# Performance work log

Hardware: AMD Instinct MI355X
Metric: run time of the kernel (lower is better)

The kernel has to match this reference:

```python
import jax, jax.numpy as jnp
import numpy as np

B, T, I, H = 64, 512, 512, 1024


def setup_inputs() -> dict:
    key = jax.random.key(0)
    ks = jax.random.split(key, 14)
    s = 0.05
    d = {"x": jax.random.normal(ks[0], (B, T, I), dtype=jnp.float32)}
    names = ["W_i", "W_f", "W_c", "W_o"]
    for n, k in zip(names, ks[1:5]):
        d[n] = jax.random.normal(k, (H, I), dtype=jnp.float32) * s
    for n, k in zip(["U_i", "U_f", "U_c", "U_o"], ks[5:9]):
        d[n] = jax.random.normal(k, (H, H), dtype=jnp.float32) * s
    for n, k in zip(["b_i", "b_f", "b_c", "b_o"], ks[9:13]):
        d[n] = jax.random.normal(k, (H,), dtype=jnp.float32) * s
    return d


def _lstm(x, W_i, W_f, W_c, W_o, b_i, b_f, b_c, b_o, U_i, U_f, U_c, U_o):
    # Precompute all input-gate preactivations in big GEMMs: (B,T,H)
    xi = jnp.einsum("bti,hi->bth", x, W_i) + b_i
    xf = jnp.einsum("bti,hi->bth", x, W_f) + b_f
    xg = jnp.einsum("bti,hi->bth", x, W_c) + b_c
    xo = jnp.einsum("bti,hi->bth", x, W_o) + b_o
    # time-major for scan: (T,B,H)
    xs = (xi.transpose(1, 0, 2), xf.transpose(1, 0, 2),
          xg.transpose(1, 0, 2), xo.transpose(1, 0, 2))
    h0 = jnp.zeros((x.shape[0], U_i.shape[0]), dtype=x.dtype)
    c0 = jnp.zeros_like(h0)

    def step(carry, xt):
        h, c = carry
        xi_t, xf_t, xg_t, xo_t = xt
        i = jax.nn.sigmoid(xi_t + h @ U_i.T)
        f = jax.nn.sigmoid(xf_t + h @ U_f.T)
        g = jnp.tanh(xg_t + h @ U_c.T)
        o = jax.nn.sigmoid(xo_t + h @ U_o.T)
        c_n = f * c + i * g
        h_n = o * jnp.tanh(c_n)
        return (h_n, c_n), h_n

    (h_n, c_n), ys = jax.lax.scan(step, (h0, c0), xs)
    out = ys.transpose(1, 0, 2)  # (B,T,H), batch_first
    return out, h_n, c_n


def reference(x, W_i, W_f, W_c, W_o, U_i, U_f, U_c, U_o, b_i, b_f, b_c, b_o):
    return _lstm(x, W_i, W_f, W_c, W_o, b_i, b_f, b_c, b_o, U_i, U_f, U_c, U_o)
```

## Files before the change

kernel.cpp:

```cpp
#include <hip/hip_runtime.h>
#include <hip/hip_bf16.h>


typedef __attribute__((ext_vector_type(8))) short bf16x8;
typedef __attribute__((ext_vector_type(4))) float f32x4;
typedef unsigned int uint32;

static __device__ __forceinline__ unsigned short f2bf(float f) {
    union { float f; unsigned int u; } v; v.f = f;
    unsigned int r = v.u + 0x7fffu + ((v.u >> 16) & 1u);
    return (unsigned short)(r >> 16);
}

#define NB   64
#define NT   512
#define NI   512
#define NH   1024
#define NWG  64


__global__ void prep_fast(const float* __restrict__ x,
                          const float* __restrict__ Wi, const float* __restrict__ Wf,
                          const float* __restrict__ Wc, const float* __restrict__ Wo,
                          unsigned short* __restrict__ Wb, unsigned short* __restrict__ xTb,
                          uint32* __restrict__ hb, int* __restrict__ arr)
{
    const int NW  = 4 * NH * NI;
    const int NX  = NB * NT * NI;
    const int NHB = 2 * NB * (NH / 2);
    const int total = NW + NX + NHB + NT;
    for (int idx = blockIdx.x * blockDim.x + threadIdx.x; idx < total;
         idx += gridDim.x * blockDim.x) {
        if (idx < NW) {
            int g = idx >> 19;
            int off = idx & 524287;
            const float* W = (g == 0) ? Wi : (g == 1) ? Wf : (g == 2) ? Wc : Wo;
            Wb[idx] = f2bf(W[off]);
        } else if (idx < NW + NX) {
            int e = idx - NW;
            int b = e >> 18;
            int r = e & 262143;
            int t = r >> 9;
            int i = r & 511;
            xTb[((size_t)t * NB + b) * NI + i] = f2bf(x[e]);
        } else if (idx < NW + NX + NHB) {
            hb[idx - NW - NX] = 0;
        } else {
            arr[idx - NW - NX - NHB] = 0;
        }
    }
}

__global__ __launch_bounds__(1024) void lstm_persist(
    const float* __restrict__ Ui, const float* __restrict__ Uf,
    const float* __restrict__ Uc, const float* __restrict__ Uo,
    const float* __restrict__ b_i, const float* __restrict__ b_f,
    const float* __restrict__ b_c, const float* __restrict__ b_o,
    const unsigned short* __restrict__ Wb, const unsigned short* __restrict__ xT,
    uint32* __restrict__ hb0, uint32* __restrict__ hb1,
    int* __restrict__ arr,
    float* __restrict__ out, float* __restrict__ hn_arr, float* __restrict__ cn_arr)
{
    __shared__ __align__(16) unsigned char smem[163840];
    unsigned char* Us   = smem;
    unsigned char* stg0 = smem + 131072;
    unsigned char* stg1 = smem + 147456;
    float* gacc = (float*)(smem + 131072);

    const int tid  = threadIdx.x;
    const int lane = tid & 63;
    const int wv   = tid >> 6;
    const int g    = wv & 3;
    const int mt   = wv >> 2;
    const int rm   = lane & 15;
    const int kg   = (lane >> 4) * 8;
    const int u0   = blockIdx.x * 16;

    for (int i = 0; i < 8; ++i) {
        int unit = i * 1024 + tid;
        int row  = unit >> 7;
        int k0   = (unit & 127) * 8;
        int gg   = row >> 4;
        const float* src = (gg == 0 ? Ui : gg == 1 ? Uf : gg == 2 ? Uc : Uo)
                           + (size_t)(u0 + (row & 15)) * NH + k0;
        bf16x8 v;
        #pragma unroll
        for (int j = 0; j < 8; ++j) v[j] = (short)f2bf(src[j]);
        *(bf16x8*)(Us + row * 2048 + ((k0 * 2) ^ ((row & 15) << 4))) = v;
    }

    const int bl = tid >> 4, ul = tid & 15;
    const float rbi = b_i[u0 + ul], rbf = b_f[u0 + ul];
    const float rbc = b_c[u0 + ul], rbo = b_o[u0 + ul];
    float creg = 0.f;

    const int sb   = bl;
    const int k8   = ul * 8;
    const int soff = sb * 256 + ((k8 * 2) ^ ((sb & 15) << 4));
    const size_t hrow = (size_t)sb * (NH / 2);

    const int abase = (mt * 16 + rm) * 256;
    const int ubase = (g * 16 + rm) * 2048;
    const size_t wrow = ((size_t)(g * NH + u0 + rm)) * NI;

    __syncthreads();

    for (int t = 0; t < NT; ++t) {
        const uint32* hin = (t & 1) ? hb1 : hb0;
        uint32* hout      = (t & 1) ? hb0 : hb1;
        const unsigned short* xrow = xT + ((size_t)t * NB + sb) * NI;

        f32x4 acc = {0.f, 0.f, 0.f, 0.f};
        uint32 rr[4][4];

        #pragma unroll
        for (int c = 0; c < 4; ++c) {
            uint32* hp = (uint32*)(hin + hrow + (c * 128 + k8) / 2);
            #pragma unroll
            for (int j = 0; j < 4; ++j)
                rr[c][j] = __hip_atomic_load(hp + j, __ATOMIC_RELAXED,
                                             __HIP_MEMORY_SCOPE_AGENT);
        }
        {
            uint4 v; v.x = rr[0][0]; v.y = rr[0][1]; v.z = rr[0][2]; v.w = rr[0][3];
            *(uint4*)(stg0 + soff) = v;
        }
        __syncthreads();

        #pragma unroll
        for (int c = 0; c < 12; ++c) {
            if (c + 4 < 12) {
                const int cc = c + 4;
                if (cc < 8) {
                    uint32* hp = (uint32*)(hin + hrow + (cc * 128 + k8) / 2);
                    #pragma unroll
                    for (int j = 0; j < 4; ++j)
                        rr[cc & 3][j] = __hip_atomic_load(hp + j, __ATOMIC_RELAXED,
                                                          __HIP_MEMORY_SCOPE_AGENT);
                } else {
                    const uint4 v = *(const uint4*)(xrow + (cc - 8) * 128 + k8);
                    rr[cc & 3][0] = v.x; rr[cc & 3][1] = v.y;
                    rr[cc & 3][2] = v.z; rr[cc & 3][3] = v.w;
                }
            }
            const unsigned char* sbuf = (c & 1) ? stg1 : stg0;
            #pragma unroll
            for (int kk = 0; kk < 4; ++kk) {
                const int kloc = kk * 32 + kg;
                bf16x8 af = *(const bf16x8*)(sbuf + abase + ((kloc * 2) ^ (rm << 4)));
                bf16x8 bfg;
                if (c < 8) {
                    const int kglob = c * 128 + kloc;
                    bfg = *(const bf16x8*)(Us + ubase + ((kglob * 2) ^ (rm << 4)));
                } else {
                    bfg = *(const bf16x8*)(Wb + wrow + (c - 8) * 128 + kloc);
                }
                acc = __builtin_amdgcn_mfma_f32_16x16x32_bf16(af, bfg, acc, 0, 0, 0);
            }
            if (c + 1 < 12) {
                unsigned char* dbuf = ((c + 1) & 1) ? stg1 : stg0;
                uint4 v; v.x = rr[(c + 1) & 3][0]; v.y = rr[(c + 1) & 3][1];
                v.z = rr[(c + 1) & 3][2]; v.w = rr[(c + 1) & 3][3];
                *(uint4*)(dbuf + soff) = v;
            }
            __syncthreads();
        }

        #pragma unroll
        for (int r = 0; r < 4; ++r) {
            const int brow = mt * 16 + (lane >> 4) * 4 + r;
            gacc[(g * 64 + brow) * 16 + rm] = acc[r];
        }
        __syncthreads();

        {
            float pi = gacc[(0 * 64 + bl) * 16 + ul] + rbi;
            float pf = gacc[(1 * 64 + bl) * 16 + ul] + rbf;
            float pg = gacc[(2 * 64 + bl) * 16 + ul] + rbc;
            float po = gacc[(3 * 64 + bl) * 16 + ul] + rbo;
            float ig  = 1.f / (1.f + __expf(-pi));
            float fg  = 1.f / (1.f + __expf(-pf));
            float gg2 = tanhf(pg);
            float og  = 1.f / (1.f + __expf(-po));
            float cn2 = fg * creg + ig * gg2;
            float hn2 = og * tanhf(cn2);
            creg = cn2;
            out[((size_t)bl * NT + t) * NH + u0 + ul] = hn2;
            unsigned short h16 = f2bf(hn2);
            unsigned int other = ((unsigned int)__shfl_xor((int)h16, 1, 64)) & 0xffffu;
            if (!(ul & 1)) {
                uint32 pk = (uint32)h16 | (other << 16);
                __hip_atomic_store(hout + hrow + (u0 + ul) / 2, pk,
                                   __ATOMIC_RELAXED, __HIP_MEMORY_SCOPE_AGENT);
            }
            if (t == NT - 1) {
                hn_arr[(size_t)bl * NH + u0 + ul] = hn2;
                cn_arr[(size_t)bl * NH + u0 + ul] = cn2;
            }
        }

        __syncthreads();
        if (tid == 0) {
            __hip_atomic_fetch_add(&arr[t], 1, __ATOMIC_RELAXED,
                                   __HIP_MEMORY_SCOPE_AGENT);
            while (__hip_atomic_load(&arr[t], __ATOMIC_RELAXED,
                                     __HIP_MEMORY_SCOPE_AGENT) < NWG)
                __builtin_amdgcn_s_sleep(1);
        }
        __syncthreads();
    }
}


__global__ void lstm_prep(const float* __restrict__ Ui, const float* __restrict__ Uf,
                          const float* __restrict__ Uc, const float* __restrict__ Uo,
                          const float* __restrict__ Wi, const float* __restrict__ Wf,
                          const float* __restrict__ Wc, const float* __restrict__ Wo,
                          unsigned short* __restrict__ Ub, unsigned short* __restrict__ Wb,
                          unsigned short* __restrict__ hb0, float* __restrict__ c_state)
{
    const int NU = 4 * NH * NH;
    const int NW = 4 * NH * NI;
    const int NS = NB * NH;
    const int total = NU + NW + NS + NS;
    for (int idx = blockIdx.x * blockDim.x + threadIdx.x; idx < total;
         idx += gridDim.x * blockDim.x) {
        if (idx < NU) {
            int g = idx >> 20;
            int off = idx & (NH * NH - 1);
            const float* U = (g == 0) ? Ui : (g == 1) ? Uf : (g == 2) ? Uc : Uo;
            Ub[idx] = f2bf(U[off]);
        } else if (idx < NU + NW) {
            int j = idx - NU;
            int g = j >> 19;
            int off = j & (NH * NI - 1);
            const float* W = (g == 0) ? Wi : (g == 1) ? Wf : (g == 2) ? Wc : Wo;
            Wb[j] = f2bf(W[off]);
        } else if (idx < NU + NW + NS) {
            hb0[idx - NU - NW] = 0;
        } else {
            c_state[idx - NU - NW - NS] = 0.0f;
        }
    }
}

__global__ __launch_bounds__(256) void lstm_step(
    const float* __restrict__ x,
    const unsigned short* __restrict__ Ub,
    const unsigned short* __restrict__ Wb,
    const unsigned short* __restrict__ hb_in,
    unsigned short* __restrict__ hb_out,
    const float* __restrict__ bi, const float* __restrict__ bff,
    const float* __restrict__ bc, const float* __restrict__ bo,
    float* __restrict__ out, float* __restrict__ c_state,
    float* __restrict__ hn_out, int t)
{
    __shared__ float gacc[4][32][16];
    const int lane = threadIdx.x & 63;
    const int g    = threadIdx.x >> 6;
    const int u0   = (blockIdx.x >> 1) * 16;
    const int b0   = (blockIdx.x & 1) * 32;
    const int rm   = lane & 15;
    const int kg   = (lane >> 4) * 8;

    f32x4 acc0 = {0.f, 0.f, 0.f, 0.f};
    f32x4 acc1 = {0.f, 0.f, 0.f, 0.f};

    const unsigned short* Ug  = Ub + (size_t)g * (NH * NH) + (size_t)(u0 + rm) * NH;
    const unsigned short* h0p = hb_in + (size_t)(b0 + rm) * NH;
    const unsigned short* h1p = hb_in + (size_t)(b0 + 16 + rm) * NH;
    #pragma unroll 4
    for (int k0 = 0; k0 < NH; k0 += 32) {
        bf16x8 bfrag = *(const bf16x8*)(Ug + k0 + kg);
        bf16x8 a0 = *(const bf16x8*)(h0p + k0 + kg);
        bf16x8 a1 = *(const bf16x8*)(h1p + k0 + kg);
        acc0 = __builtin_amdgcn_mfma_f32_16x16x32_bf16(a0, bfrag, acc0, 0, 0, 0);
        acc1 = __builtin_amdgcn_mfma_f32_16x16x32_bf16(a1, bfrag, acc1, 0, 0, 0);
    }
    const unsigned short* Wg  = Wb + (size_t)g * (NH * NI) + (size_t)(u0 + rm) * NI;
    const float* x0p = x + ((size_t)(b0 + rm) * NT + t) * NI;
    const float* x1p = x + ((size_t)(b0 + 16 + rm) * NT + t) * NI;
    #pragma unroll 2
    for (int k0 = 0; k0 < NI; k0 += 32) {
        bf16x8 bfrag = *(const bf16x8*)(Wg + k0 + kg);
        f32x4 lo0 = *(const f32x4*)(x0p + k0 + kg);
        f32x4 hi0 = *(const f32x4*)(x0p + k0 + kg + 4);
        f32x4 lo1 = *(const f32x4*)(x1p + k0 + kg);
        f32x4 hi1 = *(const f32x4*)(x1p + k0 + kg + 4);
        bf16x8 a0, a1;
        #pragma unroll
        for (int j = 0; j < 4; j++) {
            a0[j]     = (short)f2bf(lo0[j]);
            a0[j + 4] = (short)f2bf(hi0[j]);
            a1[j]     = (short)f2bf(lo1[j]);
            a1[j + 4] = (short)f2bf(hi1[j]);
        }
        acc0 = __builtin_amdgcn_mfma_f32_16x16x32_bf16(a0, bfrag, acc0, 0, 0, 0);
        acc1 = __builtin_amdgcn_mfma_f32_16x16x32_bf16(a1, bfrag, acc1, 0, 0, 0);
    }
    const int row4 = (lane >> 4) * 4;
    #pragma unroll
    for (int r = 0; r < 4; r++) {
        gacc[g][row4 + r][rm]      = acc0[r];
        gacc[g][16 + row4 + r][rm] = acc1[r];
    }
    __syncthreads();
    for (int p = threadIdx.x; p < 512; p += 256) {
        int bl = p >> 4, ul = p & 15;
        int b = b0 + bl, u = u0 + ul;
        float pi = gacc[0][bl][ul] + bi[u];
        float pf = gacc[1][bl][ul] + bff[u];
        float pg = gacc[2][bl][ul] + bc[u];
        float po = gacc[3][bl][ul] + bo[u];
        float ig = 1.f / (1.f + __expf(-pi));
        float fg = 1.f / (1.f + __expf(-pf));
        float gg = tanhf(pg);
        float og = 1.f / (1.f + __expf(-po));
        float cold = c_state[(size_t)b * NH + u];
        float cn = fg * cold + ig * gg;
        float hn = og * tanhf(cn);
        c_state[(size_t)b * NH + u] = cn;
        out[((size_t)b * NT + t) * NH + u] = hn;
        hb_out[(size_t)b * NH + u] = f2bf(hn);
        if (hn_out) hn_out[(size_t)b * NH + u] = hn;
    }
}


extern "C" void kernel_launch(void* const* d_in, const int* in_sizes, int n_in,
                              void* d_out, int out_size, void* d_ws, size_t ws_size,
                              hipStream_t stream) {
    const float* x  = (const float*)d_in[0];
    const float* Wi = (const float*)d_in[1];
    const float* Wf = (const float*)d_in[2];
    const float* Wc = (const float*)d_in[3];
    const float* Wo = (const float*)d_in[4];
    const float* Ui = (const float*)d_in[5];
    const float* Uf = (const float*)d_in[6];
    const float* Uc = (const float*)d_in[7];
    const float* Uo = (const float*)d_in[8];
    const float* bi = (const float*)d_in[9];
    const float* bf = (const float*)d_in[10];
    const float* bc = (const float*)d_in[11];
    const float* bo = (const float*)d_in[12];

    float* out = (float*)d_out;
    float* hn  = out + (size_t)NB * NT * NH;
    float* cn  = hn + (size_t)NB * NH;

    const size_t NEED = 38012928ULL;
    if (ws_size >= NEED) {
        char* ws = (char*)d_ws;
        unsigned short* Wb = (unsigned short*)ws;
        unsigned short* xT = (unsigned short*)(ws + 4194304);
        uint32* hb0 = (uint32*)(ws + 37748736);
        uint32* hb1 = (uint32*)(ws + 37748736 + 131072);
        int* arr    = (int*)(ws + 38010880);
        prep_fast<<<2048, 256, 0, stream>>>(x, Wi, Wf, Wc, Wo, Wb, xT, hb0, arr);
        lstm_persist<<<NWG, 1024, 0, stream>>>(Ui, Uf, Uc, Uo, bi, bf, bc, bo,
                                               Wb, xT, hb0, hb1, arr, out, hn, cn);
    } else {
        char* ws = (char*)d_ws;
        unsigned short* Ub  = (unsigned short*)ws;
        unsigned short* Wb  = (unsigned short*)(ws + 8388608);
        unsigned short* hb0 = (unsigned short*)(ws + 12582912);
        unsigned short* hb1 = (unsigned short*)(ws + 12713984);
        float* c_state = cn;
        lstm_prep<<<1024, 256, 0, stream>>>(Ui, Uf, Uc, Uo, Wi, Wf, Wc, Wo,
                                            Ub, Wb, hb0, c_state);
        for (int t = 0; t < NT; t++) {
            unsigned short* hin  = (t & 1) ? hb1 : hb0;
            unsigned short* hout = (t & 1) ? hb0 : hb1;
            lstm_step<<<128, 256, 0, stream>>>(
                x, Ub, Wb, hin, hout, bi, bf, bc, bo,
                out, c_state, (t == NT - 1) ? hn : (float*)nullptr, t);
        }
    }
}
```

Measured before the change: 8.246 ms.

## Replace global counter barrier with per-workgroup flags and overlap input GEMM before wait

Each workgroup now computes the input-projection MFMA part (x·W) for step t before waiting on the previous step's hidden state. It then waits only on per-producer flags (one wave polls 64 padded flags) instead of an atomic counter barrier at the end of each step. The hidden state moves to a triple-buffered bf16 array written as 64-bit packed stores. This takes the x-projection work off the serial critical path and removes atomic contention on a shared counter. In exchange it needs a larger flags array in the workspace and adds a bounded spin that could time out without error.

```diff
diff --git a/kernel.cpp b/kernel.cpp
--- a/kernel.cpp
+++ b/kernel.cpp
@@ -5,6 +5,7 @@
 typedef __attribute__((ext_vector_type(8))) short bf16x8;
 typedef __attribute__((ext_vector_type(4))) float f32x4;
 typedef unsigned int uint32;
+typedef unsigned long long u64;
 
 static __device__ __forceinline__ unsigned short f2bf(float f) {
     union { float f; unsigned int u; } v; v.f = f;
@@ -19,16 +20,16 @@
 #define NWG  64
 
 
-__global__ void prep_fast(const float* __restrict__ x,
-                          const float* __restrict__ Wi, const float* __restrict__ Wf,
-                          const float* __restrict__ Wc, const float* __restrict__ Wo,
-                          unsigned short* __restrict__ Wb, unsigned short* __restrict__ xTb,
-                          uint32* __restrict__ hb, int* __restrict__ arr)
+__global__ void prep3(const float* __restrict__ x,
+                      const float* __restrict__ Wi, const float* __restrict__ Wf,
+                      const float* __restrict__ Wc, const float* __restrict__ Wo,
+                      unsigned short* __restrict__ Wb, unsigned short* __restrict__ xTb,
+                      int* __restrict__ flags)
 {
-    const int NW  = 4 * NH * NI;
-    const int NX  = NB * NT * NI;
-    const int NHB = 2 * NB * (NH / 2);
-    const int total = NW + NX + NHB + NT;
+    const int NW = 4 * NH * NI;
+    const int NX = NB * NT * NI;
+    const int NF = NT * 1024;
+    const int total = NW + NX + NF;
     for (int idx = blockIdx.x * blockDim.x + threadIdx.x; idx < total;
          idx += gridDim.x * blockDim.x) {
         if (idx < NW) {
@@ -43,22 +44,20 @@
             int t = r >> 9;
             int i = r & 511;
             xTb[((size_t)t * NB + b) * NI + i] = f2bf(x[e]);
-        } else if (idx < NW + NX + NHB) {
-            hb[idx - NW - NX] = 0;
         } else {
-            arr[idx - NW - NX - NHB] = 0;
-        }
-    }
-}
-
-__global__ __launch_bounds__(1024) void lstm_persist(
+            flags[idx - NW - NX] = 0;
+        }
+    }
+}
+
+__global__ __launch_bounds__(1024) void lstm_persist3(
     const float* __restrict__ Ui, const float* __restrict__ Uf,
     const float* __restrict__ Uc, const float* __restrict__ Uo,
     const float* __restrict__ b_i, const float* __restrict__ b_f,
     const float* __restrict__ b_c, const float* __restrict__ b_o,
     const unsigned short* __restrict__ Wb, const unsigned short* __restrict__ xT,
-    uint32* __restrict__ hb0, uint32* __restrict__ hb1,
-    int* __restrict__ arr,
+    unsigned short* __restrict__ hb,
+    int* __restrict__ flags,
     float* __restrict__ out, float* __restrict__ hn_arr, float* __restrict__ cn_arr)
 {
     __shared__ __align__(16) unsigned char smem[163840];
@@ -74,7 +73,8 @@
     const int mt   = wv >> 2;
     const int rm   = lane & 15;
     const int kg   = (lane >> 4) * 8;
-    const int u0   = blockIdx.x * 16;
+    const int wg   = blockIdx.x;
+    const int u0   = wg * 16;
 
     for (int i = 0; i < 8; ++i) {
         int unit = i * 1024 + tid;
@@ -97,7 +97,6 @@
     const int sb   = bl;
     const int k8   = ul * 8;
     const int soff = sb * 256 + ((k8 * 2) ^ ((sb & 15) << 4));
-    const size_t hrow = (size_t)sb * (NH / 2);
 
     const int abase = (mt * 16 + rm) * 256;
     const int ubase = (g * 16 + rm) * 2048;
@@ -106,64 +105,80 @@
     __syncthreads();
 
     for (int t = 0; t < NT; ++t) {
-        const uint32* hin = (t & 1) ? hb1 : hb0;
-        uint32* hout      = (t & 1) ? hb0 : hb1;
+        f32x4 acc = {0.f, 0.f, 0.f, 0.f};
+
         const unsigned short* xrow = xT + ((size_t)t * NB + sb) * NI;
-
-        f32x4 acc = {0.f, 0.f, 0.f, 0.f};
-        uint32 rr[4][4];
-
+        uint4 xr[4];
+        #pragma unroll
+        for (int c = 0; c < 4; ++c)
+            xr[c] = *(const uint4*)(xrow + c * 128 + k8);
+        *(uint4*)(stg0 + soff) = xr[0];
+        __syncthreads();
         #pragma unroll
         for (int c = 0; c < 4; ++c) {
-            uint32* hp = (uint32*)(hin + hrow + (c * 128 + k8) / 2);
-            #pragma unroll
-            for (int j = 0; j < 4; ++j)
-                rr[c][j] = __hip_atomic_load(hp + j, __ATOMIC_RELAXED,
-                                             __HIP_MEMORY_SCOPE_AGENT);
-        }
-        {
-            uint4 v; v.x = rr[0][0]; v.y = rr[0][1]; v.z = rr[0][2]; v.w = rr[0][3];
-            *(uint4*)(stg0 + soff) = v;
-        }
-        __syncthreads();
-
-        #pragma unroll
-        for (int c = 0; c < 12; ++c) {
-            if (c + 4 < 12) {
-                const int cc = c + 4;
-                if (cc < 8) {
-                    uint32* hp = (uint32*)(hin + hrow + (cc * 128 + k8) / 2);
-                    #pragma unroll
-                    for (int j = 0; j < 4; ++j)
-                        rr[cc & 3][j] = __hip_atomic_load(hp + j, __ATOMIC_RELAXED,
-                                                          __HIP_MEMORY_SCOPE_AGENT);
-                } else {
-                    const uint4 v = *(const uint4*)(xrow + (cc - 8) * 128 + k8);
-                    rr[cc & 3][0] = v.x; rr[cc & 3][1] = v.y;
-                    rr[cc & 3][2] = v.z; rr[cc & 3][3] = v.w;
-                }
-            }
             const unsigned char* sbuf = (c & 1) ? stg1 : stg0;
             #pragma unroll
             for (int kk = 0; kk < 4; ++kk) {
                 const int kloc = kk * 32 + kg;
                 bf16x8 af = *(const bf16x8*)(sbuf + abase + ((kloc * 2) ^ (rm << 4)));
-                bf16x8 bfg;
-                if (c < 8) {
+                bf16x8 bw = *(const bf16x8*)(Wb + wrow + c * 128 + kloc);
+                acc = __builtin_amdgcn_mfma_f32_16x16x32_bf16(af, bw, acc, 0, 0, 0);
+            }
+            if (c < 3) {
+                unsigned char* dbuf = ((c + 1) & 1) ? stg1 : stg0;
+                *(uint4*)(dbuf + soff) = xr[c + 1];
+            }
+            __syncthreads();
+        }
+
+        if (t > 0) {
+            if (wv == 0) {
+                const int* fp = flags + (size_t)(t - 1) * 1024 + lane * 16;
+                int spins = 0;
+                while (__hip_atomic_load(fp, __ATOMIC_RELAXED,
+                                         __HIP_MEMORY_SCOPE_AGENT) == 0 &&
+                       spins < (1 << 20)) {
+                    __builtin_amdgcn_s_sleep(2);
+                    ++spins;
+                }
+            }
+            __syncthreads();
+
+            const u64* hsrc = (const u64*)hb + (size_t)((t - 1) % 3) * 16384
+                              + (size_t)sb * 256 + (size_t)ul * 2;
+            u64 hr[8][2];
+            #pragma unroll
+            for (int c = 0; c < 8; ++c) {
+                hr[c][0] = __hip_atomic_load(hsrc + c * 32, __ATOMIC_RELAXED,
+                                             __HIP_MEMORY_SCOPE_AGENT);
+                hr[c][1] = __hip_atomic_load(hsrc + c * 32 + 1, __ATOMIC_RELAXED,
+                                             __HIP_MEMORY_SCOPE_AGENT);
+            }
+            {
+                uint4 v; v.x = (uint32)hr[0][0]; v.y = (uint32)(hr[0][0] >> 32);
+                v.z = (uint32)hr[0][1]; v.w = (uint32)(hr[0][1] >> 32);
+                *(uint4*)(stg0 + soff) = v;
+            }
+            __syncthreads();
+            #pragma unroll
+            for (int c = 0; c < 8; ++c) {
+                const unsigned char* sbuf = (c & 1) ? stg1 : stg0;
+                #pragma unroll
+                for (int kk = 0; kk < 4; ++kk) {
+                    const int kloc = kk * 32 + kg;
+                    bf16x8 af = *(const bf16x8*)(sbuf + abase + ((kloc * 2) ^ (rm << 4)));
                     const int kglob = c * 128 + kloc;
-                    bfg = *(const bf16x8*)(Us + ubase + ((kglob * 2) ^ (rm << 4)));
-                } else {
-                    bfg = *(const bf16x8*)(Wb + wrow + (c - 8) * 128 + kloc);
+                    bf16x8 bu = *(const bf16x8*)(Us + ubase + ((kglob * 2) ^ (rm << 4)));
+                    acc = __builtin_amdgcn_mfma_f32_16x16x32_bf16(af, bu, acc, 0, 0, 0);
                 }
-                acc = __builtin_amdgcn_mfma_f32_16x16x32_bf16(af, bfg, acc, 0, 0, 0);
-            }
-            if (c + 1 < 12) {
-                unsigned char* dbuf = ((c + 1) & 1) ? stg1 : stg0;
-                uint4 v; v.x = rr[(c + 1) & 3][0]; v.y = rr[(c + 1) & 3][1];
-                v.z = rr[(c + 1) & 3][2]; v.w = rr[(c + 1) & 3][3];
-                *(uint4*)(dbuf + soff) = v;
-            }
-            __syncthreads();
+                if (c < 7) {
+                    unsigned char* dbuf = ((c + 1) & 1) ? stg1 : stg0;
+                    uint4 v; v.x = (uint32)hr[c + 1][0]; v.y = (uint32)(hr[c + 1][0] >> 32);
+                    v.z = (uint32)hr[c + 1][1]; v.w = (uint32)(hr[c + 1][1] >> 32);
+                    *(uint4*)(dbuf + soff) = v;
+                }
+                __syncthreads();
+            }
         }
 
         #pragma unroll
@@ -186,12 +201,16 @@
             float hn2 = og * tanhf(cn2);
             creg = cn2;
             out[((size_t)bl * NT + t) * NH + u0 + ul] = hn2;
+
             unsigned short h16 = f2bf(hn2);
-            unsigned int other = ((unsigned int)__shfl_xor((int)h16, 1, 64)) & 0xffffu;
-            if (!(ul & 1)) {
-                uint32 pk = (uint32)h16 | (other << 16);
-                __hip_atomic_store(hout + hrow + (u0 + ul) / 2, pk,
-                                   __ATOMIC_RELAXED, __HIP_MEMORY_SCOPE_AGENT);
+            uint32 lo = (uint32)h16 |
+                        ((((uint32)__shfl_down((int)h16, 1, 64)) & 0xffffu) << 16);
+            u64 p4 = (u64)lo | ((u64)(uint32)__shfl_down((int)lo, 2, 64) << 32);
+            if ((ul & 3) == 0) {
+                u64* hd = (u64*)hb + (size_t)(t % 3) * 16384
+                          + (size_t)bl * 256 + (size_t)((u0 + ul) >> 2);
+                __hip_atomic_store(hd, p4, __ATOMIC_RELAXED,
+                                   __HIP_MEMORY_SCOPE_AGENT);
             }
             if (t == NT - 1) {
                 hn_arr[(size_t)bl * NH + u0 + ul] = hn2;
@@ -200,14 +219,9 @@
         }
 
         __syncthreads();
-        if (tid == 0) {
-            __hip_atomic_fetch_add(&arr[t], 1, __ATOMIC_RELAXED,
-                                   __HIP_MEMORY_SCOPE_AGENT);
-            while (__hip_atomic_load(&arr[t], __ATOMIC_RELAXED,
-                                     __HIP_MEMORY_SCOPE_AGENT) < NWG)
-                __builtin_amdgcn_s_sleep(1);
-        }
-        __syncthreads();
+        if (tid == 0)
+            __hip_atomic_store(flags + (size_t)t * 1024 + wg * 16, 1,
+                               __ATOMIC_RELAXED, __HIP_MEMORY_SCOPE_AGENT);
     }
 }
 
@@ -348,17 +362,16 @@
     float* hn  = out + (size_t)NB * NT * NH;
     float* cn  = hn + (size_t)NB * NH;
 
-    const size_t NEED = 38012928ULL;
-    if (ws_size >= NEED) {
+    const size_t NEED3 = 40239104ULL;
+    if (ws_size >= NEED3) {
         char* ws = (char*)d_ws;
         unsigned short* Wb = (unsigned short*)ws;
         unsigned short* xT = (unsigned short*)(ws + 4194304);
-        uint32* hb0 = (uint32*)(ws + 37748736);
-        uint32* hb1 = (uint32*)(ws + 37748736 + 131072);
-        int* arr    = (int*)(ws + 38010880);
-        prep_fast<<<2048, 256, 0, stream>>>(x, Wi, Wf, Wc, Wo, Wb, xT, hb0, arr);
-        lstm_persist<<<NWG, 1024, 0, stream>>>(Ui, Uf, Uc, Uo, bi, bf, bc, bo,
-                                               Wb, xT, hb0, hb1, arr, out, hn, cn);
+        unsigned short* hb = (unsigned short*)(ws + 37748736);
+        int* flags         = (int*)(ws + 38141952);
+        prep3<<<2048, 256, 0, stream>>>(x, Wi, Wf, Wc, Wo, Wb, xT, flags);
+        lstm_persist3<<<NWG, 1024, 0, stream>>>(Ui, Uf, Uc, Uo, bi, bf, bc, bo,
+                                                Wb, xT, hb, flags, out, hn, cn);
     } else {
         char* ws = (char*)d_ws;
         unsigned short* Ub  = (unsigned short*)ws;
```

New measurement: 6.838 ms. -17.1%, faster.
